# Performance work log

Measured on AMD Instinct MI355X. Metric: run time of the kernel, lower is better.

## Reference

```python
import jax, jax.numpy as jnp
import numpy as np

N_DATASETS = 2
DATASET_CATS = (1536, 1536)
TOTAL_CATS = 3072
MAX_UNIFY = 1536
N_NODES = TOTAL_CATS + MAX_UNIFY  # 4608
LRELU_ALPHA = 0.2
BI_TEMP = 0.05
NEG_INF = -9e15


def setup_inputs() -> dict:
    key = jax.random.key(0)
    ks = jax.random.split(key, 12)
    nfeat, nfeat_out, nfeat_adj, nhid, nheads = 512, 256, 64, 64, 4
    att_out, mlp = 256, 512
    s = lambda k, sh: (jax.random.normal(k, sh, jnp.float32) * 0.05)
    return {
        'x': jax.random.normal(ks[0], (N_NODES, nfeat), jnp.float32),
        'W_before': s(ks[1], (nfeat, nfeat_out)),
        'b_before': jnp.zeros((nfeat_out,), jnp.float32),
        'W_adj': s(ks[2], (nfeat_out, nfeat_adj)),
        'b_adj': jnp.zeros((nfeat_adj,), jnp.float32),
        'W_heads': s(ks[3], (nheads, nfeat_out, nhid)),
        'a_heads': s(ks[4], (nheads, 2 * nhid)),
        'W_out': s(ks[5], (nheads * nhid, att_out)),
        'a_out': s(ks[6], (2 * att_out,)),
        'W_lin1': s(ks[7], (att_out, mlp)),
        'b_lin1': jnp.zeros((mlp,), jnp.float32),
    }


def _calc_adjacency(x_out, W_adj, b_adj):
    # linear_adj + L2 normalize + cosine similarity + row normalization via diag(1/rowsum)
    af = x_out @ W_adj + b_adj                              # [N, nfeat_adj]
    nrm = jnp.sqrt(jnp.sum(af * af, axis=1, keepdims=True))
    naf = af / jnp.maximum(nrm, 1e-12)
    sim = naf @ naf.T                                       # [N, N]
    rowsum = jnp.sum(sim, axis=1)
    r_inv = 1.0 / rowsum
    r_inv = jnp.where(jnp.isinf(r_inv), 0.0, r_inv)
    return r_inv[:, None] * sim                             # diag(1/rowsum) @ sim


def _gat_multihead(x, adj, W, a):
    # W: [H, F, d], a: [H, 2d]. Standard pyGAT dense attention, vectorized over heads.
    d = W.shape[-1]
    Wh = jnp.einsum('nf,hfd->hnd', x, W)                    # [H, N, d]
    f1 = jnp.einsum('hnd,hd->hn', Wh, a[:, :d])             # [H, N]
    f2 = jnp.einsum('hnd,hd->hn', Wh, a[:, d:])             # [H, N]
    e = jax.nn.leaky_relu(f1[:, :, None] + f2[:, None, :], LRELU_ALPHA)  # [H, N, N]
    att = jnp.where(adj[None] > 0, e, NEG_INF)
    att = jax.nn.softmax(att, axis=-1)
    return jnp.einsum('hnm,hmd->hnd', att, Wh)              # [H, N, d]


def _gat_single(x, adj, W, a):
    d = W.shape[-1]
    Wh = x @ W                                              # [N, d]
    f1 = Wh @ a[:d]
    f2 = Wh @ a[d:]
    e = jax.nn.leaky_relu(f1[:, None] + f2[None, :], LRELU_ALPHA)
    att = jnp.where(adj > 0, e, NEG_INF)
    att = jax.nn.softmax(att, axis=-1)
    return att @ Wh


def reference(x, W_before, b_before, W_adj, b_adj, W_heads, a_heads, W_out, a_out, W_lin1, b_lin1):
    x1 = x @ W_before + b_before                            # linear_before
    adj = _calc_adjacency(x1, W_adj, b_adj)                 # before relu, as in source
    x1 = jax.nn.relu(x1)
    # multi-head GAT layer 1 (concat=True -> elu per head, concat along feature dim)
    h = jax.nn.elu(_gat_multihead(x1, adj, W_heads, a_heads))   # [H, N, d]
    H, N, d = h.shape
    feat = jnp.transpose(h, (1, 0, 2)).reshape(N, H * d)
    x2 = feat + x1                                          # residual; dropout is eval no-op
    # output attention head (concat=False -> no elu inside)
    x3 = jax.nn.elu(_gat_single(x2, adj, W_out, a_out) + x2)
    feat_mlp = x3 @ W_lin1 + b_lin1                          # linear1
    # sep_bipartite_graphs: per-dataset column-softmax over unify columns
    bgs = []
    cur = 0
    for nc in DATASET_CATS:
        blk = adj[cur:cur + nc, TOTAL_CATS:]                 # [nc, MAX_UNIFY]
        bgs.append(jax.nn.softmax(blk / BI_TEMP, axis=0))
        cur += nc
    return (feat_mlp[TOTAL_CATS:],) + tuple(bgs)


if __name__ == '__main__':
    out = reference(**setup_inputs())
    for o in out:
        print(o.shape, o.dtype)
```

## Files before the change

kernel.cpp:

```cpp
#include <hip/hip_runtime.h>
#include <hip/hip_bf16.h>
#include <math.h>

constexpr int NTOT = 4608;
constexpr int TC   = 3072;
constexpr int MU   = 1536;
constexpr int NH   = 4;

constexpr long OFF_ADJ  = 0;
constexpr long OFF_X1   = OFF_ADJ  + (long)NTOT*NTOT;
constexpr long OFF_NAF  = OFF_X1   + (long)NTOT*256;
constexpr long OFF_PART = OFF_NAF  + (long)NTOT*64;
constexpr long OFF_RINV = OFF_PART + 72*64;
constexpr long OFF_WH   = OFF_RINV + NTOT;
constexpr long OFF_F1H  = OFF_WH   + (long)4*NTOT*64;
constexpr long OFF_F2H  = OFF_F1H  + (long)4*NTOT;
constexpr long OFF_MXH  = OFF_F2H  + (long)4*NTOT;
constexpr long OFF_CIH  = OFF_MXH  + (long)4*NTOT;
constexpr long OFF_X2   = OFF_CIH  + (long)4*NTOT;
constexpr long OFF_WH2  = OFF_X2   + (long)NTOT*256;
constexpr long OFF_F1S  = OFF_WH2  + (long)NTOT*256;
constexpr long OFF_F2S  = OFF_F1S  + NTOT;
constexpr long OFF_MXS  = OFF_F2S  + NTOT;
constexpr long OFF_CIS  = OFF_MXS  + NTOT;
constexpr long OFF_X3   = OFF_CIS  + NTOT;
constexpr long OFF_PMAX = OFF_X3   + (long)MU*256;
constexpr long OFF_PSUM = OFF_PMAX + (long)2*12*MU;
constexpr long OFF_FMAX = OFF_PSUM + (long)2*12*MU;
constexpr long OFF_FIS  = OFF_FMAX + (long)2*MU;
constexpr long OFF_L1   = OFF_FIS  + (long)2*MU;
constexpr long OFF_L2   = OFF_L1   + (long)4*NTOT;
constexpr long OFF_PARTS = OFF_ADJ + (long)TC*NTOT;
constexpr long OFF_POSB  = OFF_PARTS + 2L*NTOT*36;
constexpr long OFF_MASKB = OFF_POSB  + 2L*NTOT*72;
constexpr long OFF_PM2   = OFF_MASKB + 2L*NTOT*72;
constexpr long OFF_PS2   = OFF_PM2   + 2L*96*MU;

typedef __attribute__((ext_vector_type(8))) short bf16x8;
typedef __attribute__((ext_vector_type(8))) unsigned short ushort8;
typedef __attribute__((ext_vector_type(4))) float floatx4;

__device__ __forceinline__ float elu(float x)   { return (x > 0.f) ? x : expm1f(x); }
__device__ __forceinline__ unsigned short f2bf(float f) {
    unsigned u = __float_as_uint(f);
    u += 0x7FFFu + ((u >> 16) & 1u);
    return (unsigned short)(u >> 16);
}

__global__ __launch_bounds__(256) void zero2_k(
    float* __restrict__ a, long na4, float* __restrict__ b, long nb4)
{
    long i = (long)blockIdx.x * 256 + threadIdx.x;
    float4 z = make_float4(0.f, 0.f, 0.f, 0.f);
    if (i < na4) *(float4*)(a + i * 4) = z;
    else {
        long j = i - na4;
        if (j < nb4) *(float4*)(b + j * 4) = z;
    }
}

template<bool RELU_A, bool BIAS>
__global__ __launch_bounds__(256) void gemm_rm(
    const float* __restrict__ A, const float* __restrict__ B,
    const float* __restrict__ bias, float* __restrict__ C,
    int K, int M, long strideBz, long strideCz)
{
    __shared__ float As[16][68];
    __shared__ float Bs[16][68];
    const float* Bz = B + (long)blockIdx.z * strideBz;
    float* Cz = C + (long)blockIdx.z * strideCz;
    int tid = threadIdx.x;
    int r0 = blockIdx.x * 64;
    int c0 = blockIdx.y * 64;
    int ty = tid >> 4, tx = tid & 15;
    int srow = tid >> 2, skg = tid & 3;
    int bkk = tid >> 4, bc4 = (tid & 15) * 4;
    const float* Arow = A + (long)(r0 + srow) * K + skg * 4;
    float4 aReg = *(const float4*)(Arow);
    float4 bReg = *(const float4*)&Bz[(long)bkk * M + c0 + bc4];
    float acc[4][4] = {};
    for (int k0 = 0; k0 < K; k0 += 16) {
        {
            float4 v = aReg;
            if (RELU_A) {
                v.x = fmaxf(v.x, 0.f); v.y = fmaxf(v.y, 0.f);
                v.z = fmaxf(v.z, 0.f); v.w = fmaxf(v.w, 0.f);
            }
            As[skg * 4 + 0][srow] = v.x;
            As[skg * 4 + 1][srow] = v.y;
            As[skg * 4 + 2][srow] = v.z;
            As[skg * 4 + 3][srow] = v.w;
            *(float4*)&Bs[bkk][bc4] = bReg;
        }
        __syncthreads();
        if (k0 + 16 < K) {
            aReg = *(const float4*)(Arow + k0 + 16);
            bReg = *(const float4*)&Bz[(long)(k0 + 16 + bkk) * M + c0 + bc4];
        }
        #pragma unroll
        for (int kk = 0; kk < 16; ++kk) {
            float4 av = *(const float4*)&As[kk][ty * 4];
            float4 bv = *(const float4*)&Bs[kk][tx * 4];
            float a[4] = { av.x, av.y, av.z, av.w };
            float b[4] = { bv.x, bv.y, bv.z, bv.w };
            #pragma unroll
            for (int i = 0; i < 4; ++i)
                #pragma unroll
                for (int j = 0; j < 4; ++j) acc[i][j] += a[i] * b[j];
        }
        __syncthreads();
    }
    #pragma unroll
    for (int i = 0; i < 4; ++i) {
        int r = r0 + ty * 4 + i;
        #pragma unroll
        for (int j = 0; j < 4; ++j) {
            int c = c0 + tx * 4 + j;
            float v = acc[i][j];
            if (BIAS) v += bias[c];
            Cz[(long)r * M + c] = v;
        }
    }
}

__global__ __launch_bounds__(256) void af_naf(
    const float* __restrict__ x1, const float* __restrict__ W_adj,
    const float* __restrict__ b_adj, float* __restrict__ nafT)
{
    __shared__ float rowbuf[4][256];
    int tid = threadIdx.x, w = tid >> 6, lane = tid & 63;
    int n = blockIdx.x * 4 + w;
    #pragma unroll
    for (int l = 0; l < 4; ++l) rowbuf[w][l * 64 + lane] = x1[(long)n * 256 + l * 64 + lane];
    __syncthreads();
    float acc = b_adj[lane];
    for (int k = 0; k < 256; ++k) acc += rowbuf[w][k] * W_adj[k * 64 + lane];
    float sq = acc * acc;
    #pragma unroll
    for (int off = 32; off >= 1; off >>= 1) sq += __shfl_xor(sq, off);
    float nrm = fmaxf(sqrtf(sq), 1e-12f);
    nafT[(long)lane * NTOT + n] = acc / nrm;
}

__global__ __launch_bounds__(256) void sim_k8(
    const float* __restrict__ nafT, float* __restrict__ sim,
    double* __restrict__ parts, unsigned long long* __restrict__ posb)
{
    __shared__ float As[32][128];
    __shared__ float Bs[32][128];
    __shared__ unsigned char sgn[128][2][16];
    int tid = threadIdx.x;
    int n0 = blockIdx.x * 128, m0 = blockIdx.y * 128;
    int ty = tid >> 4, tx = tid & 15;
    float acc[2][2][4][4] = {};
    for (int ks = 0; ks < 2; ++ks) {
        if (ks) __syncthreads();
        int k0 = ks * 32;
        #pragma unroll
        for (int l = 0; l < 4; ++l) {
            int idx = l * 256 + tid;
            int kk = idx >> 5, f4 = idx & 31;
            *(float4*)&As[kk][f4 * 4] = *(const float4*)&nafT[(long)(k0 + kk) * NTOT + n0 + f4 * 4];
            *(float4*)&Bs[kk][f4 * 4] = *(const float4*)&nafT[(long)(k0 + kk) * NTOT + m0 + f4 * 4];
        }
        __syncthreads();
        for (int kk = 0; kk < 32; ++kk) {
            float4 av0 = *(const float4*)&As[kk][ty * 4];
            float4 av1 = *(const float4*)&As[kk][64 + ty * 4];
            float4 bv0 = *(const float4*)&Bs[kk][tx * 4];
            float4 bv1 = *(const float4*)&Bs[kk][64 + tx * 4];
            float a[2][4] = { { av0.x, av0.y, av0.z, av0.w }, { av1.x, av1.y, av1.z, av1.w } };
            float b[2][4] = { { bv0.x, bv0.y, bv0.z, bv0.w }, { bv1.x, bv1.y, bv1.z, bv1.w } };
            #pragma unroll
            for (int rh = 0; rh < 2; ++rh)
                #pragma unroll
                for (int ch = 0; ch < 2; ++ch)
                    #pragma unroll
                    for (int i = 0; i < 4; ++i)
                        #pragma unroll
                        for (int j = 0; j < 4; ++j)
                            acc[rh][ch][i][j] += a[rh][i] * b[ch][j];
        }
    }
    if (m0 >= TC && n0 < TC) {
        #pragma unroll
        for (int rh = 0; rh < 2; ++rh)
            #pragma unroll
            for (int i = 0; i < 4; ++i) {
                long r = n0 + rh * 64 + ty * 4 + i;
                #pragma unroll
                for (int ch = 0; ch < 2; ++ch) {
                    float4 o = make_float4(acc[rh][ch][i][0], acc[rh][ch][i][1],
                                           acc[rh][ch][i][2], acc[rh][ch][i][3]);
                    *(float4*)(sim + r * NTOT + m0 + ch * 64 + tx * 4) = o;
                }
            }
    }
    int mt36 = m0 >> 7;
    #pragma unroll
    for (int rh = 0; rh < 2; ++rh)
        #pragma unroll
        for (int i = 0; i < 4; ++i) {
            double t = 0.0;
            #pragma unroll
            for (int ch = 0; ch < 2; ++ch)
                t += ((double)acc[rh][ch][i][0] + (double)acc[rh][ch][i][1])
                   + ((double)acc[rh][ch][i][2] + (double)acc[rh][ch][i][3]);
            #pragma unroll
            for (int off = 1; off < 16; off <<= 1) t += __shfl_xor(t, off);
            if (tx == 0)
                parts[(long)(n0 + rh * 64 + ty * 4 + i) * 36 + mt36] = t;
        }
    int mt = m0 >> 6;
    #pragma unroll
    for (int rh = 0; rh < 2; ++rh)
        #pragma unroll
        for (int i = 0; i < 4; ++i)
            #pragma unroll
            for (int ch = 0; ch < 2; ++ch) {
                unsigned nib = (unsigned)(acc[rh][ch][i][0] > 0.f)
                             | ((unsigned)(acc[rh][ch][i][1] > 0.f) << 1)
                             | ((unsigned)(acc[rh][ch][i][2] > 0.f) << 2)
                             | ((unsigned)(acc[rh][ch][i][3] > 0.f) << 3);
                sgn[rh * 64 + ty * 4 + i][ch][tx] = (unsigned char)nib;
            }
    __syncthreads();
    {
        int rl = tid >> 1, gh = tid & 1;
        unsigned long long w = 0;
        #pragma unroll
        for (int t = 0; t < 16; ++t)
            w |= (unsigned long long)sgn[rl][gh][t] << (4 * t);
        posb[(long)(n0 + rl) * 72 + mt + gh] = w;
    }
}

__global__ __launch_bounds__(256) void fused1(
    const float* __restrict__ Wh, unsigned short* __restrict__ Whbf,
    const float* __restrict__ a_heads,
    float* __restrict__ f1, float* __restrict__ f2,
    const double* __restrict__ parts, const unsigned long long* __restrict__ posb,
    float* __restrict__ rinv, unsigned long long* __restrict__ maskT)
{
    __shared__ float t[64][65];
    int b = blockIdx.x;
    int tid = threadIdx.x;
    if (b < 288) {
        int bx = b % 72, bz = b / 72;
        int n0 = bx * 64;
        const float* inz = Wh + (long)bz * NTOT * 64;
        unsigned short* outz = Whbf + (long)bz * 64 * NTOT;
        int r4 = tid >> 6, k = tid & 63;
        #pragma unroll
        for (int l = 0; l < 16; ++l) {
            int row = l * 4 + r4;
            t[row][k] = inz[(long)(n0 + row) * 64 + k];
        }
        __syncthreads();
        #pragma unroll
        for (int l = 0; l < 16; ++l) {
            int drow = l * 4 + r4;
            outz[(long)drow * NTOT + n0 + k] = f2bf(t[k][drow]);
        }
    } else if (b < 288 + 4608) {
        int tb = b - 288;
        int xb = tb % 1152, h = tb / 1152;
        int w = tid >> 6, lane = tid & 63;
        int n = xb * 4 + w;
        const float* row = Wh + ((long)h * NTOT + n) * 64;
        const float* a1 = a_heads + (long)h * 128;
        const float* a2 = a1 + 64;
        float v = row[lane];
        float p1 = v * a1[lane];
        float p2 = v * a2[lane];
        #pragma unroll
        for (int off = 32; off >= 1; off >>= 1) { p1 += __shfl_xor(p1, off); p2 += __shfl_xor(p2, off); }
        if (lane == 0) {
            f1[(long)h * NTOT + n] = p1;
            f2[(long)h * NTOT + n] = p2;
        }
    } else {
        int xb = b - (288 + 4608);
        int w = tid >> 6, lane = tid & 63;
        int n = xb * 4 + w;
        double s = (lane < 36) ? parts[(long)n * 36 + lane] : 0.0;
        #pragma unroll
        for (int off = 32; off >= 1; off >>= 1) s += __shfl_xor(s, off);
        float rs = (float)s;
        float r = 1.0f / rs;
        if (isinf(r)) r = 0.f;
        if (lane == 0) rinv[n] = r;
        unsigned long long pw = posb[(long)n * 72 + lane];
        unsigned long long mw = (r < 0.f) ? ~pw : pw;
        if (r == 0.f) mw = 0ull;
        maskT[(long)lane * NTOT + n] = mw;
        if (lane < 8) {
            pw = posb[(long)n * 72 + 64 + lane];
            mw = (r < 0.f) ? ~pw : pw;
            if (r == 0.f) mw = 0ull;
            maskT[(long)(64 + lane) * NTOT + n] = mw;
        }
    }
}

__global__ __launch_bounds__(256) void fused2(
    const float* __restrict__ Wh2, unsigned short* __restrict__ Wh2bf,
    const float* __restrict__ a_out,
    float* __restrict__ f1, float* __restrict__ f2)
{
    __shared__ float t[64][65];
    int b = blockIdx.x;
    int tid = threadIdx.x;
    if (b < 288) {
        int bx = b % 72, by = b / 72;
        int n0 = bx * 64, d0 = by * 64;
        int r4 = tid >> 6, k = tid & 63;
        #pragma unroll
        for (int l = 0; l < 16; ++l) {
            int row = l * 4 + r4;
            t[row][k] = Wh2[(long)(n0 + row) * 256 + d0 + k];
        }
        __syncthreads();
        #pragma unroll
        for (int l = 0; l < 16; ++l) {
            int drow = l * 4 + r4;
            Wh2bf[(long)(d0 + drow) * NTOT + n0 + k] = f2bf(t[k][drow]);
        }
    } else {
        int xb = b - 288;
        int w = tid >> 6, lane = tid & 63;
        int n = xb * 4 + w;
        const float* row = Wh2 + (long)n * 256;
        const float* a1 = a_out;
        const float* a2 = a_out + 256;
        float p1 = 0.f, p2 = 0.f;
        #pragma unroll
        for (int l = 0; l < 4; ++l) {
            float v = row[l * 64 + lane];
            p1 += v * a1[l * 64 + lane];
            p2 += v * a2[l * 64 + lane];
        }
        #pragma unroll
        for (int off = 32; off >= 1; off >>= 1) { p1 += __shfl_xor(p1, off); p2 += __shfl_xor(p2, off); }
        if (lane == 0) {
            f1[n] = p1;
            f2[n] = p2;
        }
    }
}

__global__ __launch_bounds__(256) void mh_attn(
    const unsigned long long* __restrict__ maskT,
    const float* __restrict__ f1, const float* __restrict__ f2,
    const unsigned short* __restrict__ Whbf, float* __restrict__ accb,
    float* __restrict__ lbuf)
{
    __shared__ unsigned short Ws[2][64][72];
    int tid = threadIdx.x;
    int wave = tid >> 6, lane = tid & 63;
    int n0 = blockIdx.x * 64;
    int h = blockIdx.y, ch = blockIdx.z;
    const float* f2h = f2 + (long)h * NTOT;
    const unsigned short* Wb = Whbf + (long)h * 64 * NTOT;
    int wd = tid >> 2, wc = (tid & 3) * 16;
    int arow = lane & 15, acol8 = (lane >> 4) * 8;
    int n = n0 + 16 * wave + arow;
    float r1 = f1[(long)h * NTOT + n];
    float lsum = 0.f;
    floatx4 acc[4] = {};
    int buf = 0;
    int mt0 = ch * 12;
    ushort8 wv0 = *(const ushort8*)&Wb[(long)wd * NTOT + mt0 * 64 + wc];
    ushort8 wv1 = *(const ushort8*)&Wb[(long)wd * NTOT + mt0 * 64 + wc + 8];
    unsigned long long mw = maskT[(long)mt0 * NTOT + n];
    for (int i = 0; i < 12; ++i) {
        int m0 = (mt0 + i) * 64;
        bf16x8 afr[2];
        #pragma unroll
        for (int ks = 0; ks < 2; ++ks) {
            int mc = m0 + ks * 32 + acol8;
            float4 fv0 = *(const float4*)(f2h + mc);
            float4 fv1 = *(const float4*)(f2h + mc + 4);
            unsigned bits = (unsigned)(mw >> (ks * 32 + acol8)) & 0xFFu;
            float f[8] = { fv0.x, fv0.y, fv0.z, fv0.w, fv1.x, fv1.y, fv1.z, fv1.w };
            #pragma unroll
            for (int j = 0; j < 8; ++j) {
                float s = r1 + f[j];
                float e = __expf(fmaxf(s, 0.2f * s));
                float p = ((bits >> j) & 1u) ? e : 0.f;
                lsum += p;
                afr[ks][j] = (short)f2bf(p);
            }
        }
        *(ushort8*)&Ws[buf][wd][wc] = wv0;
        *(ushort8*)&Ws[buf][wd][wc + 8] = wv1;
        if (i < 11) {
            int m1 = (mt0 + i + 1) * 64;
            wv0 = *(const ushort8*)&Wb[(long)wd * NTOT + m1 + wc];
            wv1 = *(const ushort8*)&Wb[(long)wd * NTOT + m1 + wc + 8];
            mw = maskT[(long)(mt0 + i + 1) * NTOT + n];
        }
        __syncthreads();
        #pragma unroll
        for (int ks = 0; ks < 2; ++ks) {
            #pragma unroll
            for (int dt = 0; dt < 4; ++dt) {
                bf16x8 bfr = *(bf16x8*)&Ws[buf][16 * dt + arow][ks * 32 + acol8];
                acc[dt] = __builtin_amdgcn_mfma_f32_16x16x32_bf16(afr[ks], bfr, acc[dt], 0, 0, 0);
            }
        }
        buf ^= 1;
    }
    lsum += __shfl_xor(lsum, 16);
    lsum += __shfl_xor(lsum, 32);
    if (lane < 16) atomicAdd(lbuf + (long)h * NTOT + n0 + 16 * wave + lane, lsum);
    int crow = n0 + 16 * wave + (lane >> 4) * 4;
    int ccol = h * 64 + (lane & 15);
    #pragma unroll
    for (int dt = 0; dt < 4; ++dt)
        #pragma unroll
        for (int r = 0; r < 4; ++r)
            atomicAdd(accb + (long)(crow + r) * 256 + ccol + dt * 16, acc[dt][r]);
}

__global__ __launch_bounds__(256) void mh_fin(
    const float* __restrict__ accb, const float* __restrict__ lbuf,
    float* __restrict__ x1, float* __restrict__ x2)
{
    long idx = ((long)blockIdx.x * 256 + threadIdx.x) * 4;
    long r = idx >> 8;
    int h = (int)((idx & 255) >> 6);
    float l = lbuf[(long)h * NTOT + r];
    float inv = (l > 0.f) ? 1.0f / l : 0.f;
    float4 a = *(const float4*)(accb + idx);
    float4 xv = *(const float4*)(x1 + idx);
    float4 o;
    o.x = elu(a.x * inv) + fmaxf(xv.x, 0.f);
    o.y = elu(a.y * inv) + fmaxf(xv.y, 0.f);
    o.z = elu(a.z * inv) + fmaxf(xv.z, 0.f);
    o.w = elu(a.w * inv) + fmaxf(xv.w, 0.f);
    *(float4*)(x2 + idx) = o;
    if (idx < (long)MU * 256)
        *(float4*)(x1 + idx) = make_float4(0.f, 0.f, 0.f, 0.f);
}

__global__ __launch_bounds__(256) void s_attn(
    const unsigned long long* __restrict__ maskT,
    const float* __restrict__ f1, const float* __restrict__ f2,
    const unsigned short* __restrict__ Wh2bf, float* __restrict__ accb,
    float* __restrict__ lbuf)
{
    __shared__ unsigned short Ws[2][128][72];
    int tid = threadIdx.x;
    int wave = tid >> 6, lane = tid & 63;
    int lr0 = blockIdx.x * 32;
    int c0 = blockIdx.y * 128;
    int ch = blockIdx.z;
    int wdl = tid >> 2, wc = (tid & 3) * 16;
    int arow = lane & 15, acol8 = (lane >> 4) * 8;
    int rt = wave & 1;
    int dt0 = (wave >> 1) * 4;
    int n = TC + lr0 + 16 * rt + arow;
    float r1 = f1[n];
    float lsum = 0.f;
    floatx4 acc[4] = {};
    int buf = 0;
    int mt0 = ch * 6;
    ushort8 wva0 = *(const ushort8*)&Wh2bf[(long)(c0 + wdl) * NTOT + mt0 * 64 + wc];
    ushort8 wva1 = *(const ushort8*)&Wh2bf[(long)(c0 + wdl) * NTOT + mt0 * 64 + wc + 8];
    ushort8 wvb0 = *(const ushort8*)&Wh2bf[(long)(c0 + 64 + wdl) * NTOT + mt0 * 64 + wc];
    ushort8 wvb1 = *(const ushort8*)&Wh2bf[(long)(c0 + 64 + wdl) * NTOT + mt0 * 64 + wc + 8];
    unsigned long long mw = maskT[(long)mt0 * NTOT + n];
    for (int i = 0; i < 6; ++i) {
        int m0 = (mt0 + i) * 64;
        bf16x8 afr[2];
        #pragma unroll
        for (int ks = 0; ks < 2; ++ks) {
            int mc = m0 + ks * 32 + acol8;
            float4 fv0 = *(const float4*)(f2 + mc);
            float4 fv1 = *(const float4*)(f2 + mc + 4);
            unsigned bits = (unsigned)(mw >> (ks * 32 + acol8)) & 0xFFu;
            float f[8] = { fv0.x, fv0.y, fv0.z, fv0.w, fv1.x, fv1.y, fv1.z, fv1.w };
            #pragma unroll
            for (int j = 0; j < 8; ++j) {
                float s = r1 + f[j];
                float e = __expf(fmaxf(s, 0.2f * s));
                float p = ((bits >> j) & 1u) ? e : 0.f;
                lsum += p;
                afr[ks][j] = (short)f2bf(p);
            }
        }
        *(ushort8*)&Ws[buf][wdl][wc] = wva0;
        *(ushort8*)&Ws[buf][wdl][wc + 8] = wva1;
        *(ushort8*)&Ws[buf][64 + wdl][wc] = wvb0;
        *(ushort8*)&Ws[buf][64 + wdl][wc + 8] = wvb1;
        if (i < 5) {
            int m1 = (mt0 + i + 1) * 64;
            wva0 = *(const ushort8*)&Wh2bf[(long)(c0 + wdl) * NTOT + m1 + wc];
            wva1 = *(const ushort8*)&Wh2bf[(long)(c0 + wdl) * NTOT + m1 + wc + 8];
            wvb0 = *(const ushort8*)&Wh2bf[(long)(c0 + 64 + wdl) * NTOT + m1 + wc];
            wvb1 = *(const ushort8*)&Wh2bf[(long)(c0 + 64 + wdl) * NTOT + m1 + wc + 8];
            mw = maskT[(long)(mt0 + i + 1) * NTOT + n];
        }
        __syncthreads();
        #pragma unroll
        for (int ks = 0; ks < 2; ++ks) {
            #pragma unroll
            for (int t = 0; t < 4; ++t) {
                bf16x8 bfr = *(bf16x8*)&Ws[buf][(dt0 + t) * 16 + arow][ks * 32 + acol8];
                acc[t] = __builtin_amdgcn_mfma_f32_16x16x32_bf16(afr[ks], bfr, acc[t], 0, 0, 0);
            }
        }
        buf ^= 1;
    }
    lsum += __shfl_xor(lsum, 16);
    lsum += __shfl_xor(lsum, 32);
    if (blockIdx.y == 0 && wave < 2 && lane < 16)
        atomicAdd(lbuf + lr0 + 16 * wave + lane, lsum);
    int crow = lr0 + 16 * rt + (lane >> 4) * 4;
    #pragma unroll
    for (int t = 0; t < 4; ++t) {
        int ccol = c0 + (dt0 + t) * 16 + (lane & 15);
        #pragma unroll
        for (int r = 0; r < 4; ++r)
            atomicAdd(accb + (long)(crow + r) * 256 + ccol, acc[t][r]);
    }
}

__global__ __launch_bounds__(256) void s_fin(
    const float* __restrict__ accb, const float* __restrict__ lbuf,
    const float* __restrict__ x2, float* __restrict__ x3)
{
    long idx = ((long)blockIdx.x * 256 + threadIdx.x) * 4;
    long r = idx >> 8;
    float l = lbuf[r];
    float inv = (l > 0.f) ? 1.0f / l : 0.f;
    float4 a = *(const float4*)(accb + idx);
    float4 xv = *(const float4*)(x2 + (long)TC * 256 + idx);
    float4 o;
    o.x = elu(a.x * inv + xv.x);
    o.y = elu(a.y * inv + xv.y);
    o.z = elu(a.z * inv + xv.z);
    o.w = elu(a.w * inv + xv.w);
    *(float4*)(x3 + idx) = o;
}

__global__ __launch_bounds__(256) void bi_partial(
    const float* __restrict__ sim, const float* __restrict__ rinv,
    float* __restrict__ pmax, float* __restrict__ psum)
{
    int c = blockIdx.x * 256 + threadIdx.x;
    int ch = blockIdx.y;
    int ds = blockIdx.z;
    float m = -3.0e38f, s = 0.f;
    int rbase = ds * MU + ch * 16;
    for (int r = 0; r < 16; ++r) {
        float a = sim[(long)(rbase + r) * NTOT + TC + c] * rinv[rbase + r];
        float v = a * 20.0f;
        if (v <= m) s += expf(v - m);
        else { s = s * expf(m - v) + 1.f; m = v; }
    }
    pmax[((long)ds * 96 + ch) * MU + c] = m;
    psum[((long)ds * 96 + ch) * MU + c] = s;
}

__global__ __launch_bounds__(256) void bi_combine(
    const float* __restrict__ pmax, const float* __restrict__ psum,
    float* __restrict__ fmax, float* __restrict__ fis)
{
    int b = blockIdx.x;
    int ds = b / 6, ct = b % 6;
    int c = ct * 256 + threadIdx.x;
    float m = -3.0e38f;
    for (int ch = 0; ch < 96; ++ch) m = fmaxf(m, pmax[((long)ds * 96 + ch) * MU + c]);
    float s = 0.f;
    for (int ch = 0; ch < 96; ++ch)
        s += psum[((long)ds * 96 + ch) * MU + c] * expf(pmax[((long)ds * 96 + ch) * MU + c] - m);
    fmax[ds * MU + c] = m;
    fis[ds * MU + c] = 1.0f / s;
}

__global__ __launch_bounds__(256) void bi_norm(
    const float* __restrict__ sim, const float* __restrict__ rinv,
    const float* __restrict__ fmax, const float* __restrict__ fis,
    float* __restrict__ outbg)
{
    int c = blockIdx.x * 256 + threadIdx.x;
    int ch = blockIdx.y;
    int ds = blockIdx.z;
    float m = fmax[ds * MU + c], inv = fis[ds * MU + c];
    long obase = (long)ds * MU * MU;
    int rbase = ch * 16;
    for (int r = 0; r < 16; ++r) {
        int row = ds * MU + rbase + r;
        float a = sim[(long)row * NTOT + TC + c] * rinv[row];
        float v = a * 20.0f;
        outbg[obase + (long)(rbase + r) * MU + c] = expf(v - m) * inv;
    }
}

extern "C" void kernel_launch(void* const* d_in, const int* in_sizes, int n_in,
                              void* d_out, int out_size, void* d_ws, size_t ws_size,
                              hipStream_t stream)
{
    const float* x        = (const float*)d_in[0];
    const float* W_before = (const float*)d_in[1];
    const float* b_before = (const float*)d_in[2];
    const float* W_adj    = (const float*)d_in[3];
    const float* b_adj    = (const float*)d_in[4];
    const float* W_heads  = (const float*)d_in[5];
    const float* a_heads  = (const float*)d_in[6];
    const float* W_out    = (const float*)d_in[7];
    const float* a_out    = (const float*)d_in[8];
    const float* W_lin1   = (const float*)d_in[9];
    const float* b_lin1   = (const float*)d_in[10];
    float* out = (float*)d_out;
    float* ws  = (float*)d_ws;

    float* sim  = ws + OFF_ADJ;
    float* x1p  = ws + OFF_X1;
    float* nafT = ws + OFF_NAF;
    float* rinv = ws + OFF_RINV;
    float* Wh   = ws + OFF_WH;
    float* f1h  = ws + OFF_F1H;
    float* f2h  = ws + OFF_F2H;
    float* x2   = ws + OFF_X2;
    float* Wh2  = ws + OFF_WH2;
    float* f1s  = ws + OFF_F1S;
    float* f2s  = ws + OFF_F2S;
    float* x3   = ws + OFF_X3;
    float* pmax = ws + OFF_PM2;
    float* psum = ws + OFF_PS2;
    float* fmx  = ws + OFF_FMAX;
    float* fis  = ws + OFF_FIS;
    float* l1   = ws + OFF_L1;
    float* l2   = ws + OFF_L2;
    float* acc1 = ws + OFF_WH2;
    float* acc2 = ws + OFF_X1;
    unsigned short* Whbf  = (unsigned short*)(ws + OFF_X2);
    unsigned short* Wh2bf = (unsigned short*)(ws + OFF_X1 + (long)MU * 256);
    double* parts = (double*)(ws + OFF_PARTS);
    unsigned long long* posb  = (unsigned long long*)(ws + OFF_POSB);
    unsigned long long* maskT = (unsigned long long*)(ws + OFF_MASKB);

    dim3 b256(256);

    zero2_k<<<dim3(1172), b256, 0, stream>>>(acc1, (long)NTOT * 64, l1, 5120);
    gemm_rm<false, true><<<dim3(72, 4, 1), b256, 0, stream>>>(x, W_before, b_before, x1p, 512, 256, 0, 0);
    af_naf<<<dim3(1152), b256, 0, stream>>>(x1p, W_adj, b_adj, nafT);
    sim_k8<<<dim3(36, 36), b256, 0, stream>>>(nafT, sim, parts, posb);
    gemm_rm<true, false><<<dim3(72, 1, 4), b256, 0, stream>>>(x1p, W_heads, nullptr, Wh, 256, 64,
                                                              (long)256 * 64, (long)NTOT * 64);
    fused1<<<dim3(288 + 4608 + 1152), b256, 0, stream>>>(Wh, Whbf, a_heads, f1h, f2h,
                                                         parts, posb, rinv, maskT);
    mh_attn<<<dim3(72, 4, 6), b256, 0, stream>>>(maskT, f1h, f2h, Whbf, acc1, l1);
    mh_fin<<<dim3(NTOT * 256 / 1024), b256, 0, stream>>>(acc1, l1, x1p, x2);
    gemm_rm<false, false><<<dim3(72, 4, 1), b256, 0, stream>>>(x2, W_out, nullptr, Wh2, 256, 256, 0, 0);
    fused2<<<dim3(288 + 1152), b256, 0, stream>>>(Wh2, Wh2bf, a_out, f1s, f2s);
    s_attn<<<dim3(48, 2, 12), b256, 0, stream>>>(maskT, f1s, f2s, Wh2bf, acc2, l2);
    s_fin<<<dim3(MU * 256 / 1024), b256, 0, stream>>>(acc2, l2, x2, x3);
    gemm_rm<false, true><<<dim3(24, 8, 1), b256, 0, stream>>>(x3, W_lin1, b_lin1, out, 256, 512, 0, 0);
    bi_partial<<<dim3(6, 96, 2), b256, 0, stream>>>(sim, rinv, pmax, psum);
    bi_combine<<<dim3(12), b256, 0, stream>>>(pmax, psum, fmx, fis);
    bi_norm<<<dim3(6, 96, 2), b256, 0, stream>>>(sim, rinv, fmx, fis, out + (long)MU * 512);
}
```

Before: 343.2 us.

## Double thread count in sim tile kernel and prefetch second K slab into registers

The 128x128 similarity tile kernel now runs with 512 threads instead of 256, so each thread computes a 4x8 sub-tile instead of 8x8. The second 32-wide K slab is loaded into registers while the first slab is being multiplied. This halves per-thread accumulator registers and adds waves to hide latency, at the cost of more shared-memory reads per FMA and extra barriers.

```diff
diff --git a/kernel.cpp b/kernel.cpp
--- a/kernel.cpp
+++ b/kernel.cpp
@@ -142,7 +142,7 @@
     nafT[(long)lane * NTOT + n] = acc / nrm;
 }
 
-__global__ __launch_bounds__(256) void sim_k8(
+__global__ __launch_bounds__(512) void sim_k8(
     const float* __restrict__ nafT, float* __restrict__ sim,
     double* __restrict__ parts, unsigned long long* __restrict__ posb)
 {
@@ -152,80 +152,87 @@
     int tid = threadIdx.x;
     int n0 = blockIdx.x * 128, m0 = blockIdx.y * 128;
     int ty = tid >> 4, tx = tid & 15;
-    float acc[2][2][4][4] = {};
+    float acc[2][4][4] = {};
+    float4 pa[2], pb[2];
+    #pragma unroll
+    for (int l = 0; l < 2; ++l) {
+        int idx = l * 512 + tid;
+        int kk = idx >> 5, f4 = idx & 31;
+        pa[l] = *(const float4*)&nafT[(long)kk * NTOT + n0 + f4 * 4];
+        pb[l] = *(const float4*)&nafT[(long)kk * NTOT + m0 + f4 * 4];
+    }
     for (int ks = 0; ks < 2; ++ks) {
-        if (ks) __syncthreads();
-        int k0 = ks * 32;
-        #pragma unroll
-        for (int l = 0; l < 4; ++l) {
-            int idx = l * 256 + tid;
+        #pragma unroll
+        for (int l = 0; l < 2; ++l) {
+            int idx = l * 512 + tid;
             int kk = idx >> 5, f4 = idx & 31;
-            *(float4*)&As[kk][f4 * 4] = *(const float4*)&nafT[(long)(k0 + kk) * NTOT + n0 + f4 * 4];
-            *(float4*)&Bs[kk][f4 * 4] = *(const float4*)&nafT[(long)(k0 + kk) * NTOT + m0 + f4 * 4];
+            *(float4*)&As[kk][f4 * 4] = pa[l];
+            *(float4*)&Bs[kk][f4 * 4] = pb[l];
         }
         __syncthreads();
+        if (ks == 0) {
+            #pragma unroll
+            for (int l = 0; l < 2; ++l) {
+                int idx = l * 512 + tid;
+                int kk = 32 + (idx >> 5), f4 = idx & 31;
+                pa[l] = *(const float4*)&nafT[(long)kk * NTOT + n0 + f4 * 4];
+                pb[l] = *(const float4*)&nafT[(long)kk * NTOT + m0 + f4 * 4];
+            }
+        }
         for (int kk = 0; kk < 32; ++kk) {
-            float4 av0 = *(const float4*)&As[kk][ty * 4];
-            float4 av1 = *(const float4*)&As[kk][64 + ty * 4];
+            float4 av  = *(const float4*)&As[kk][ty * 4];
             float4 bv0 = *(const float4*)&Bs[kk][tx * 4];
             float4 bv1 = *(const float4*)&Bs[kk][64 + tx * 4];
-            float a[2][4] = { { av0.x, av0.y, av0.z, av0.w }, { av1.x, av1.y, av1.z, av1.w } };
+            float a[4] = { av.x, av.y, av.z, av.w };
             float b[2][4] = { { bv0.x, bv0.y, bv0.z, bv0.w }, { bv1.x, bv1.y, bv1.z, bv1.w } };
             #pragma unroll
-            for (int rh = 0; rh < 2; ++rh)
+            for (int ch = 0; ch < 2; ++ch)
                 #pragma unroll
-                for (int ch = 0; ch < 2; ++ch)
+                for (int i = 0; i < 4; ++i)
                     #pragma unroll
-                    for (int i = 0; i < 4; ++i)
-                        #pragma unroll
-                        for (int j = 0; j < 4; ++j)
-                            acc[rh][ch][i][j] += a[rh][i] * b[ch][j];
-        }
+                    for (int j = 0; j < 4; ++j)
+                        acc[ch][i][j] += a[i] * b[ch][j];
+        }
+        if (ks == 0) __syncthreads();
     }
     if (m0 >= TC && n0 < TC) {
         #pragma unroll
-        for (int rh = 0; rh < 2; ++rh)
-            #pragma unroll
-            for (int i = 0; i < 4; ++i) {
-                long r = n0 + rh * 64 + ty * 4 + i;
-                #pragma unroll
-                for (int ch = 0; ch < 2; ++ch) {
-                    float4 o = make_float4(acc[rh][ch][i][0], acc[rh][ch][i][1],
-                                           acc[rh][ch][i][2], acc[rh][ch][i][3]);
-                    *(float4*)(sim + r * NTOT + m0 + ch * 64 + tx * 4) = o;
-                }
+        for (int i = 0; i < 4; ++i) {
+            long r = n0 + ty * 4 + i;
+            #pragma unroll
+            for (int ch = 0; ch < 2; ++ch) {
+                float4 o = make_float4(acc[ch][i][0], acc[ch][i][1],
+                                       acc[ch][i][2], acc[ch][i][3]);
+                *(float4*)(sim + r * NTOT + m0 + ch * 64 + tx * 4) = o;
             }
+        }
     }
     int mt36 = m0 >> 7;
     #pragma unroll
-    for (int rh = 0; rh < 2; ++rh)
-        #pragma unroll
-        for (int i = 0; i < 4; ++i) {
-            double t = 0.0;
-            #pragma unroll
-            for (int ch = 0; ch < 2; ++ch)
-                t += ((double)acc[rh][ch][i][0] + (double)acc[rh][ch][i][1])
-                   + ((double)acc[rh][ch][i][2] + (double)acc[rh][ch][i][3]);
-            #pragma unroll
-            for (int off = 1; off < 16; off <<= 1) t += __shfl_xor(t, off);
-            if (tx == 0)
-                parts[(long)(n0 + rh * 64 + ty * 4 + i) * 36 + mt36] = t;
-        }
+    for (int i = 0; i < 4; ++i) {
+        double t = 0.0;
+        #pragma unroll
+        for (int ch = 0; ch < 2; ++ch)
+            t += ((double)acc[ch][i][0] + (double)acc[ch][i][1])
+               + ((double)acc[ch][i][2] + (double)acc[ch][i][3]);
+        #pragma unroll
+        for (int off = 1; off < 16; off <<= 1) t += __shfl_xor(t, off);
+        if (tx == 0)
+            parts[(long)(n0 + ty * 4 + i) * 36 + mt36] = t;
+    }
     int mt = m0 >> 6;
     #pragma unroll
-    for (int rh = 0; rh < 2; ++rh)
-        #pragma unroll
-        for (int i = 0; i < 4; ++i)
-            #pragma unroll
-            for (int ch = 0; ch < 2; ++ch) {
-                unsigned nib = (unsigned)(acc[rh][ch][i][0] > 0.f)
-                             | ((unsigned)(acc[rh][ch][i][1] > 0.f) << 1)
-                             | ((unsigned)(acc[rh][ch][i][2] > 0.f) << 2)
-                             | ((unsigned)(acc[rh][ch][i][3] > 0.f) << 3);
-                sgn[rh * 64 + ty * 4 + i][ch][tx] = (unsigned char)nib;
-            }
+    for (int i = 0; i < 4; ++i)
+        #pragma unroll
+        for (int ch = 0; ch < 2; ++ch) {
+            unsigned nib = (unsigned)(acc[ch][i][0] > 0.f)
+                         | ((unsigned)(acc[ch][i][1] > 0.f) << 1)
+                         | ((unsigned)(acc[ch][i][2] > 0.f) << 2)
+                         | ((unsigned)(acc[ch][i][3] > 0.f) << 3);
+            sgn[ty * 4 + i][ch][tx] = (unsigned char)nib;
+        }
     __syncthreads();
-    {
+    if (tid < 256) {
         int rl = tid >> 1, gh = tid & 1;
         unsigned long long w = 0;
         #pragma unroll
@@ -648,7 +655,7 @@
     zero2_k<<<dim3(1172), b256, 0, stream>>>(acc1, (long)NTOT * 64, l1, 5120);
     gemm_rm<false, true><<<dim3(72, 4, 1), b256, 0, stream>>>(x, W_before, b_before, x1p, 512, 256, 0, 0);
     af_naf<<<dim3(1152), b256, 0, stream>>>(x1p, W_adj, b_adj, nafT);
-    sim_k8<<<dim3(36, 36), b256, 0, stream>>>(nafT, sim, parts, posb);
+    sim_k8<<<dim3(36, 36), dim3(512), 0, stream>>>(nafT, sim, parts, posb);
     gemm_rm<true, false><<<dim3(72, 1, 4), b256, 0, stream>>>(x1p, W_heads, nullptr, Wh, 256, 64,
                                                               (long)256 * 64, (long)NTOT * 64);
     fused1<<<dim3(288 + 4608 + 1152), b256, 0, stream>>>(Wh, Whbf, a_heads, f1h, f2h,
```

New measurement: 369.6 us. +7.7%, slower.
